# Performance work log

Hardware: AMD Instinct MI355X
Metric: run time of the kernel (lower is better)

Reference implementation:

```python
import jax, jax.numpy as jnp
import numpy as np

B, N, DIM, H, DH, P = 4, 4096, 256, 8, 64, 2
INNER = H * DH  # 512


def setup_inputs() -> dict:
    key = jax.random.key(0)
    ks = jax.random.split(key, 10)
    w = lambda k, shape: jax.random.normal(k, shape, dtype=jnp.float32) * 0.02
    return dict(
        x=jax.random.normal(ks[0], (B, N, DIM), dtype=jnp.float32),
        prev_x=jax.random.normal(ks[1], (B, N, DIM), dtype=jnp.float32),
        ln_q_g=jnp.ones((2 * DIM,), jnp.float32), ln_q_b=jnp.zeros((2 * DIM,), jnp.float32),
        ln_k_g=jnp.ones((DIM,), jnp.float32), ln_k_b=jnp.zeros((DIM,), jnp.float32),
        ln_v_g=jnp.ones((DIM,), jnp.float32), ln_v_b=jnp.zeros((DIM,), jnp.float32),
        Wq=w(ks[2], (2 * DIM, INNER)),            # to_q, bias=False
        Wk=w(ks[3], (DIM, INNER)), bk=jnp.zeros((INNER,), jnp.float32),
        Wv=w(ks[4], (DIM, INNER)), bv=jnp.zeros((INNER,), jnp.float32),
        Woff=w(ks[5], (H * P, INNER)),            # 1x1 conv == linear over channels
        boff=jax.random.uniform(ks[6], (H * P,), jnp.float32, -1.0, 1.0),
        Wout=w(ks[7], (DIM, INNER)), bout=jnp.zeros((DIM,), jnp.float32),
    )


def _ln(x, g, b):
    m = x.mean(-1, keepdims=True)
    v = ((x - m) ** 2).mean(-1, keepdims=True)
    return (x - m) * jax.lax.rsqrt(v + 1e-5) * g + b


def reference(x, prev_x, ln_q_g, ln_q_b, ln_k_g, ln_k_b, ln_v_g, ln_v_b,
              Wq, Wk, bk, Wv, bv, Woff, boff, Wout, bout):
    scale = DH ** -0.5
    # queries from cat(x, prev_x) along feature dim
    q = _ln(jnp.concatenate([x, prev_x], axis=-1), ln_q_g, ln_q_b) @ Wq  # (B,N,INNER)
    # learned per-head, per-point offsets (1x1 conv over channels)
    offsets = (q @ Woff.T + boff).reshape(B, N, H, P).transpose(0, 2, 3, 1)  # (B,H,P,N)
    # K/V from cat(x, prev_x) along batch dim -> KV length 2N per (b,h)
    kv = jnp.concatenate([x, prev_x], axis=0)  # (2B,N,DIM)
    k = (_ln(kv, ln_k_g, ln_k_b) @ Wk + bk).reshape(2, B, N, H, DH).transpose(1, 3, 4, 0, 2).reshape(B, H, DH, 2 * N)
    v = (_ln(kv, ln_v_g, ln_v_b) @ Wv + bv).reshape(2, B, N, H, DH).transpose(1, 3, 4, 0, 2).reshape(B, H, DH, 2 * N)
    # sampling positions: pos + offset, clamped, truncated to int (matches torch .long())
    pos = jnp.arange(N, dtype=jnp.float32)
    samp = jnp.clip(pos[None, None, None, :] + offsets, 0, 2 * N - 1).astype(jnp.int32)  # (B,H,P,N)
    idx = samp.transpose(0, 1, 3, 2)[:, :, None, :, :]  # (B,H,1,N,P)
    k_s = jnp.take_along_axis(k[:, :, :, None, :], idx, axis=-1)  # (B,H,DH,N,P)
    v_s = jnp.take_along_axis(v[:, :, :, None, :], idx, axis=-1)  # (B,H,DH,N,P)
    qh = q.reshape(B, N, H, DH).transpose(0, 2, 1, 3) * scale     # (B,H,N,DH)
    sim = jnp.einsum('bhnd,bhdnp->bhnp', qh, k_s)                  # (B,H,N,P)
    attn = jax.nn.softmax(sim, axis=-1)
    out = jnp.einsum('bhnp,bhdnp->bhnd', attn, v_s)                # (B,H,N,DH)
    out = out.transpose(0, 2, 1, 3).reshape(B, N, INNER) @ Wout.T + bout  # (B,N,DIM)
    return out, offsets
```

## Files before the change

### kernel.cpp

```cpp
#include <hip/hip_runtime.h>
#include <hip/hip_bf16.h>
#include <math.h>

#define B_    4
#define N_    4096
#define DIM_  256
#define H_    8
#define DH_   64
#define P_    2
#define INNER_ 512
#define BN_   (B_ * N_)
#define KVR_  (2 * BN_)

typedef short v8s  __attribute__((ext_vector_type(8)));
typedef short v4s  __attribute__((ext_vector_type(4)));
typedef float v4f  __attribute__((ext_vector_type(4)));

__device__ __forceinline__ short f2b(float x) {
    __hip_bfloat16 h = __float2bfloat16(x);
    return *reinterpret_cast<short*>(&h);
}
__device__ __forceinline__ float b2f(short s) {
    __hip_bfloat16 h = *reinterpret_cast<__hip_bfloat16*>(&s);
    return __bfloat162float(h);
}

__device__ __forceinline__ void async16(const void* g, void* l) {
    __builtin_amdgcn_global_load_lds(
        (const __attribute__((address_space(1))) void*)g,
        (__attribute__((address_space(3))) void*)l, 16, 0, 0);
}

__device__ __forceinline__ void storeRow(float* p, float4 f0, float4 f1, float4 f2, float4 f3) {
    ((float4*)p)[0] = f0; ((float4*)p)[1] = f1; ((float4*)p)[2] = f2; ((float4*)p)[3] = f3;
}
__device__ __forceinline__ void storeRow(__hip_bfloat16* p, float4 f0, float4 f1, float4 f2, float4 f3) {
    v8s o0, o1;
    o0[0]=f2b(f0.x); o0[1]=f2b(f0.y); o0[2]=f2b(f0.z); o0[3]=f2b(f0.w);
    o0[4]=f2b(f1.x); o0[5]=f2b(f1.y); o0[6]=f2b(f1.z); o0[7]=f2b(f1.w);
    o1[0]=f2b(f2.x); o1[1]=f2b(f2.y); o1[2]=f2b(f2.z); o1[3]=f2b(f2.w);
    o1[4]=f2b(f3.x); o1[5]=f2b(f3.y); o1[6]=f2b(f3.z); o1[7]=f2b(f3.w);
    ((v8s*)p)[0] = o0; ((v8s*)p)[1] = o1;
}

__global__ __launch_bounds__(256) void prep_all(
    const float* __restrict__ Wq, const float* __restrict__ gq, const float* __restrict__ betaq,
    const float* __restrict__ Wk, const float* __restrict__ gk, const float* __restrict__ betak,
    const float* __restrict__ bk,
    const float* __restrict__ Wv, const float* __restrict__ gv, const float* __restrict__ betav,
    const float* __restrict__ bv,
    const float* __restrict__ Woff, const float* __restrict__ Wout,
    short* __restrict__ Wq2t, float* __restrict__ bq2,
    short* __restrict__ Wkvt, float* __restrict__ bkv,
    float* __restrict__ Wcomb, float* __restrict__ braw, short* __restrict__ Woutb) {
    __shared__ float sm[272];
    const int bid = blockIdx.x, t = threadIdx.x;

    if (bid < 1536) {
        const float *W, *g, *beta, *bias_in;
        short* Wt; float* b2; int K, n; float scale;
        if (bid < 512)       { W=Wq; g=gq; beta=betaq; bias_in=nullptr; Wt=Wq2t; b2=bq2; K=512; n=bid;        scale=0.125f; }
        else if (bid < 1024) { W=Wk; g=gk; beta=betak; bias_in=bk; Wt=Wkvt;           b2=bkv;       K=256; n=bid-512;  scale=1.f; }
        else                 { W=Wv; g=gv; beta=betav; bias_in=bv; Wt=Wkvt+512*256;   b2=bkv+512;   K=256; n=bid-1024; scale=1.f; }
        float partial = 0.f;
        for (int k = t; k < K; k += 256) {
            float w = W[k * 512 + n];
            Wt[(size_t)n * K + k] = f2b(scale * g[k] * w);
            partial += beta[k] * w;
        }
        sm[t] = partial;
        __syncthreads();
        for (int s = 128; s > 0; s >>= 1) {
            if (t < s) sm[t] += sm[t + s];
            __syncthreads();
        }
        if (t == 0) b2[n] = scale * ((bias_in ? bias_in[n] : 0.f) + sm[0]);
    } else if (bid < 2048) {
        const int k = bid - 1536;
        const int hp = t & 15, jg = t >> 4;
        float p = 0.f;
        for (int j = jg; j < INNER_; j += 16)
            p += Wq[k * INNER_ + j] * Woff[hp * INNER_ + j];
        sm[jg * 17 + hp] = p;
        __syncthreads();
        if (t < 16) {
            float s = 0.f;
            for (int i = 0; i < 16; i++) s += sm[i * 17 + t];
            Wcomb[k * 16 + t] = gq[k] * s;
            braw[k * 16 + t]  = betaq[k] * s;
        }
    } else {
        const int i0 = (bid - 2048) * 1024 + t * 4;
        float4 f = *(const float4*)(Wout + i0);
        v4s o;
        o[0] = f2b(f.x); o[1] = f2b(f.y); o[2] = f2b(f.z); o[3] = f2b(f.w);
        *(v4s*)(Woutb + i0) = o;
    }
}

__global__ void bcomb_sum(const float* __restrict__ braw, const float* __restrict__ boff,
                          float* __restrict__ bcomb) {
    __shared__ float sm[272];
    int t = threadIdx.x;
    int hp = t & 15, kg = t >> 4;
    float p = 0.f;
    for (int k = kg; k < 512; k += 16) p += braw[k * 16 + hp];
    sm[kg * 17 + hp] = p;
    __syncthreads();
    if (t < 16) {
        float s = 0.f;
        for (int i = 0; i < 16; i++) s += sm[i * 17 + t];
        bcomb[t] = s + boff[t];
    }
}

__global__ __launch_bounds__(256) void norm_fused_kernel(
    const float* __restrict__ x, const float* __restrict__ p,
    const float* __restrict__ Wcomb, const float* __restrict__ bcomb,
    short* __restrict__ Aq, short* __restrict__ Akv,
    float* __restrict__ out_off, int* __restrict__ idx) {
    const int lane = threadIdx.x & 63;
    const int wv   = threadIdx.x >> 6;
    const int m0   = (blockIdx.x * 4 + wv) * 4;
    const int k8   = lane * 8;

    float4 w[8][4];
#pragma unroll
    for (int i = 0; i < 8; i++) {
        const float4* wr = (const float4*)(Wcomb + (size_t)(k8 + i) * 16);
#pragma unroll
        for (int j = 0; j < 4; j++) w[i][j] = wr[j];
    }
    const float bc = bcomb[lane & 15];

    const float* srcb = (lane < 32) ? (x + k8) : (p + k8 - DIM_);

    float4 u0 = ((const float4*)(srcb + (size_t)m0 * DIM_))[0];
    float4 u1 = ((const float4*)(srcb + (size_t)m0 * DIM_))[1];

#pragma unroll
    for (int r = 0; r < 4; r++) {
        const int m = m0 + r;
        float4 n0, n1;
        if (r < 3) {
            n0 = ((const float4*)(srcb + (size_t)(m + 1) * DIM_))[0];
            n1 = ((const float4*)(srcb + (size_t)(m + 1) * DIM_))[1];
        }
        float uv[8] = { u0.x, u0.y, u0.z, u0.w, u1.x, u1.y, u1.z, u1.w };

        float s = 0.f, q2 = 0.f;
#pragma unroll
        for (int i = 0; i < 8; i++) { s += uv[i]; q2 += uv[i] * uv[i]; }
#pragma unroll
        for (int d = 1; d <= 16; d <<= 1) {
            s  += __shfl_xor(s, d);
            q2 += __shfl_xor(q2, d);
        }
        float mean_h = s * (1.f / 256.f);
        float var_h  = q2 * (1.f / 256.f) - mean_h * mean_h;
        float rstd_h = rsqrtf(var_h + 1e-5f);
        float sf  = s  + __shfl_xor(s, 32);
        float q2f = q2 + __shfl_xor(q2, 32);
        float mean_q = sf * (1.f / 512.f);
        float var_q  = q2f * (1.f / 512.f) - mean_q * mean_q;
        float rstd_q = rsqrtf(var_q + 1e-5f);

        v8s okv;
#pragma unroll
        for (int i = 0; i < 8; i++) okv[i] = f2b((uv[i] - mean_h) * rstd_h);
        short* akvdst = Akv + ((lane < 32) ? ((size_t)m * DIM_ + k8)
                                           : ((size_t)(BN_ + m) * DIM_ + k8 - DIM_));
        *(v8s*)akvdst = okv;

        float nv[8];
        v8s oq;
#pragma unroll
        for (int i = 0; i < 8; i++) { nv[i] = (uv[i] - mean_q) * rstd_q; oq[i] = f2b(nv[i]); }
        *(v8s*)(Aq + (size_t)m * INNER_ + k8) = oq;

        float acc[16];
#pragma unroll
        for (int h = 0; h < 16; h++) acc[h] = 0.f;
#pragma unroll
        for (int i = 0; i < 8; i++) {
            float nvi = nv[i];
            acc[0]  += nvi * w[i][0].x;  acc[1]  += nvi * w[i][0].y;
            acc[2]  += nvi * w[i][0].z;  acc[3]  += nvi * w[i][0].w;
            acc[4]  += nvi * w[i][1].x;  acc[5]  += nvi * w[i][1].y;
            acc[6]  += nvi * w[i][1].z;  acc[7]  += nvi * w[i][1].w;
            acc[8]  += nvi * w[i][2].x;  acc[9]  += nvi * w[i][2].y;
            acc[10] += nvi * w[i][2].z;  acc[11] += nvi * w[i][2].w;
            acc[12] += nvi * w[i][3].x;  acc[13] += nvi * w[i][3].y;
            acc[14] += nvi * w[i][3].z;  acc[15] += nvi * w[i][3].w;
        }
        float a8[8];
#pragma unroll
        for (int j = 0; j < 8; j++) {
            float lo = acc[2 * j] + __shfl_xor(acc[2 * j], 1);
            float hi = acc[2 * j + 1] + __shfl_xor(acc[2 * j + 1], 1);
            a8[j] = (lane & 1) ? hi : lo;
        }
        float a4[4];
#pragma unroll
        for (int j = 0; j < 4; j++) {
            float lo = a8[2 * j] + __shfl_xor(a8[2 * j], 2);
            float hi = a8[2 * j + 1] + __shfl_xor(a8[2 * j + 1], 2);
            a4[j] = (lane & 2) ? hi : lo;
        }
        float a2[2];
#pragma unroll
        for (int j = 0; j < 2; j++) {
            float lo = a4[2 * j] + __shfl_xor(a4[2 * j], 4);
            float hi = a4[2 * j + 1] + __shfl_xor(a4[2 * j + 1], 4);
            a2[j] = (lane & 4) ? hi : lo;
        }
        float l1 = a2[0] + __shfl_xor(a2[0], 8);
        float h1 = a2[1] + __shfl_xor(a2[1], 8);
        float a1 = (lane & 8) ? h1 : l1;
        a1 += __shfl_xor(a1, 16);
        a1 += __shfl_xor(a1, 32);

        if (lane < 16) {
            float off = a1 + bc;
            int b = m >> 12, n = m & (N_ - 1);
            int h = lane >> 1, pp = lane & 1;
            out_off[(size_t)((b * H_ + h) * P_ + pp) * N_ + n] = off;
            float f = fminf(fmaxf((float)n + off, 0.f), (float)(2 * N_ - 1));
            idx[((size_t)(b * H_ + h) * N_ + n) * P_ + pp] = (int)f;
        }
        u0 = n0; u1 = n1;
    }
}

template <typename OT>
__device__ __forceinline__ void gemm_body(
    short* smem, const short* __restrict__ A, const short* __restrict__ Bt,
    const float* __restrict__ bias, OT* __restrict__ C, int N, int K, int nx, int lin) {
    short* As = smem;
    short* Bs = smem + 128 * 64;
    const int tid  = threadIdx.x;
    const int lane = tid & 63, w = tid >> 6;
    const int wr = w >> 1, wc = w & 1;
    const int lm = lane & 15, g = lane >> 4;

    const int x8 = lin & 7, t = lin >> 3;
    const int bx = t % nx, by = (t / nx) * 8 + x8;
    const int row0 = by * 128, col0 = bx * 128;

    const short* pa[4];
    const short* pb[4];
#pragma unroll
    for (int r = 0; r < 4; r++) {
        int s   = tid + 256 * r;
        int row = s >> 3, kcs = s & 7;
        int kg  = kcs ^ (row & 7);
        pa[r] = A  + (size_t)(row0 + row) * K + kg * 8;
        pb[r] = Bt + (size_t)(col0 + row) * K + kg * 8;
    }

    v4f acc[4][4];
#pragma unroll
    for (int i = 0; i < 4; i++)
#pragma unroll
        for (int j = 0; j < 4; j++) acc[i][j] = (v4f){0.f, 0.f, 0.f, 0.f};

    for (int k0 = 0; k0 < K; k0 += 64) {
        __syncthreads();
#pragma unroll
        for (int r = 0; r < 4; r++) {
            int s = tid + 256 * r;
            async16(pa[r] + k0, (char*)As + s * 16);
            async16(pb[r] + k0, (char*)Bs + s * 16);
        }
        __syncthreads();
#pragma unroll
        for (int ks = 0; ks < 2; ks++) {
            v8s af[4], bf[4];
#pragma unroll
            for (int i = 0; i < 4; i++) {
                int m   = wr * 64 + i * 16 + lm;
                int sch = m * 8 + ((ks * 4 + g) ^ (m & 7));
                af[i] = *(const v8s*)(As + sch * 8);
            }
#pragma unroll
            for (int j = 0; j < 4; j++) {
                int n   = wc * 64 + j * 16 + lm;
                int sch = n * 8 + ((ks * 4 + g) ^ (n & 7));
                bf[j] = *(const v8s*)(Bs + sch * 8);
            }
#pragma unroll
            for (int i = 0; i < 4; i++)
#pragma unroll
                for (int j = 0; j < 4; j++)
                    acc[i][j] = __builtin_amdgcn_mfma_f32_16x16x32_bf16(af[i], bf[j], acc[i][j], 0, 0, 0);
        }
    }

#pragma unroll
    for (int j = 0; j < 4; j++) {
        int gc = col0 + wc * 64 + j * 16 + lm;
        float bj = bias ? bias[gc] : 0.f;
#pragma unroll
        for (int i = 0; i < 4; i++)
#pragma unroll
            for (int r = 0; r < 4; r++) acc[i][j][r] += bj;
    }

    __syncthreads();
    float* ep = (float*)smem + w * (16 * 68);
#pragma unroll
    for (int i = 0; i < 4; i++) {
#pragma unroll
        for (int j = 0; j < 4; j++)
#pragma unroll
            for (int r = 0; r < 4; r++)
                ep[(g * 4 + r) * 68 + j * 16 + lm] = acc[i][j][r];
        asm volatile("s_waitcnt lgkmcnt(0)" ::: "memory");
        int rr = lane >> 2, cb = (lane & 3) * 16;
        float4 f0 = *(float4*)(ep + rr * 68 + cb + 0);
        float4 f1 = *(float4*)(ep + rr * 68 + cb + 4);
        float4 f2 = *(float4*)(ep + rr * 68 + cb + 8);
        float4 f3 = *(float4*)(ep + rr * 68 + cb + 12);
        asm volatile("s_waitcnt lgkmcnt(0)" ::: "memory");
        int grow = row0 + wr * 64 + i * 16 + rr;
        int gcol = col0 + wc * 64 + cb;
        storeRow(&C[(size_t)grow * N + gcol], f0, f1, f2, f3);
    }
}

__global__ __launch_bounds__(256) void gemm_qkv(
    const short* __restrict__ Aq, const short* __restrict__ Wq2t,
    const float* __restrict__ bq2, __hip_bfloat16* __restrict__ qb,
    const short* __restrict__ Akv, const short* __restrict__ Wkvt,
    const float* __restrict__ bkv, __hip_bfloat16* __restrict__ kvproj) {
    __shared__ short smem[2 * 128 * 64];
    const int bid = blockIdx.x;
    if (bid < 512)
        gemm_body<__hip_bfloat16>(smem, Aq, Wq2t, bq2, qb, 512, 512, 4, bid);
    else
        gemm_body<__hip_bfloat16>(smem, Akv, Wkvt, bkv, kvproj, 1024, 256, 8, bid - 512);
}

__global__ __launch_bounds__(256) void gemm_out(
    const short* __restrict__ A, const short* __restrict__ Bt,
    const float* __restrict__ bias, float* __restrict__ C) {
    __shared__ short smem[2 * 128 * 64];
    const int lin = blockIdx.y * gridDim.x + blockIdx.x;
    gemm_body<float>(smem, A, Bt, bias, C, 256, 512, 2, lin);
}

__global__ __launch_bounds__(256) void attn_kernel(
    const short* __restrict__ qb, const short* __restrict__ kvproj,
    const int* __restrict__ idx, short* __restrict__ attnout) {
    const int lane = threadIdx.x & 63;
    const int wv   = threadIdx.x >> 6;
    const int s    = lane >> 4, c = lane & 15;
    const int n = blockIdx.x * 16 + wv * 4 + s;
    const int h = blockIdx.y, b = blockIdx.z;
    const int m = b * N_ + n;

    v4s qv = *(const v4s*)(qb + (size_t)m * INNER_ + h * DH_ + c * 4);

    const int* ip = idx + ((size_t)(b * H_ + h) * N_ + n) * P_;
    int j0 = ip[0], j1 = ip[1];
    int r0 = b * N_ + j0 + ((j0 >= N_) ? (BN_ - N_) : 0);
    int r1 = b * N_ + j1 + ((j1 >= N_) ? (BN_ - N_) : 0);
    const short* k0p = kvproj + (size_t)r0 * 1024 + h * DH_ + c * 4;
    const short* k1p = kvproj + (size_t)r1 * 1024 + h * DH_ + c * 4;
    v4s k0 = *(const v4s*)k0p, v0 = *(const v4s*)(k0p + 512);
    v4s k1 = *(const v4s*)k1p, v1 = *(const v4s*)(k1p + 512);

    float q0 = b2f(qv[0]), q1 = b2f(qv[1]), q2 = b2f(qv[2]), q3 = b2f(qv[3]);
    float s0 = q0 * b2f(k0[0]) + q1 * b2f(k0[1]) + q2 * b2f(k0[2]) + q3 * b2f(k0[3]);
    float s1 = q0 * b2f(k1[0]) + q1 * b2f(k1[1]) + q2 * b2f(k1[2]) + q3 * b2f(k1[3]);
#pragma unroll
    for (int d = 1; d <= 8; d <<= 1) {
        s0 += __shfl_xor(s0, d);
        s1 += __shfl_xor(s1, d);
    }
    float mx = fmaxf(s0, s1);
    float e0 = __expf(s0 - mx), e1 = __expf(s1 - mx);
    float inv = 1.f / (e0 + e1);
    v4s o;
#pragma unroll
    for (int i = 0; i < 4; i++)
        o[i] = f2b((e0 * b2f(v0[i]) + e1 * b2f(v1[i])) * inv);
    *(v4s*)(attnout + (size_t)m * INNER_ + h * DH_ + c * 4) = o;
}

extern "C" void kernel_launch(void* const* d_in, const int* in_sizes, int n_in,
                              void* d_out, int out_size, void* d_ws, size_t ws_size,
                              hipStream_t stream) {
    (void)in_sizes; (void)n_in; (void)out_size; (void)ws_size;

    const float* x      = (const float*)d_in[0];
    const float* prevx  = (const float*)d_in[1];
    const float* ln_q_g = (const float*)d_in[2];
    const float* ln_q_b = (const float*)d_in[3];
    const float* ln_k_g = (const float*)d_in[4];
    const float* ln_k_b = (const float*)d_in[5];
    const float* ln_v_g = (const float*)d_in[6];
    const float* ln_v_b = (const float*)d_in[7];
    const float* Wq     = (const float*)d_in[8];
    const float* Wk     = (const float*)d_in[9];
    const float* bk     = (const float*)d_in[10];
    const float* Wv     = (const float*)d_in[11];
    const float* bv     = (const float*)d_in[12];
    const float* Woff   = (const float*)d_in[13];
    const float* boff   = (const float*)d_in[14];
    const float* Wout   = (const float*)d_in[15];
    const float* bout   = (const float*)d_in[16];

    char* cur = (char*)d_ws;
    auto alloc = [&](size_t bytes) { char* p = cur; cur += (bytes + 255) & ~(size_t)255; return p; };
    short* Aq      = (short*)alloc((size_t)BN_ * INNER_ * 2);
    short* Akv     = (short*)alloc((size_t)KVR_ * DIM_ * 2);
    short* qb      = (short*)alloc((size_t)BN_ * INNER_ * 2);
    short* kvproj  = (short*)alloc((size_t)KVR_ * 1024 * 2);
    short* attnout = (short*)alloc((size_t)BN_ * INNER_ * 2);
    short* Wq2t    = (short*)alloc(512 * 512 * 2);
    short* Wkvt    = (short*)alloc(1024 * 256 * 2);
    short* Woutb   = (short*)alloc(256 * 512 * 2);
    float* bq2     = (float*)alloc(512 * 4);
    float* bkv     = (float*)alloc(1024 * 4);
    float* Wcomb   = (float*)alloc(512 * 16 * 4);
    float* braw    = (float*)alloc(512 * 16 * 4);
    float* bcomb   = (float*)alloc(16 * 4);
    int*   idxb    = (int*)alloc((size_t)BN_ * 16 * 4);

    float* out_main = (float*)d_out;
    float* out_off  = out_main + (size_t)BN_ * DIM_;

    prep_all<<<2176, 256, 0, stream>>>(Wq, ln_q_g, ln_q_b,
                                       Wk, ln_k_g, ln_k_b, bk,
                                       Wv, ln_v_g, ln_v_b, bv,
                                       Woff, Wout,
                                       Wq2t, bq2, Wkvt, bkv, Wcomb, braw, Woutb);
    bcomb_sum<<<1, 256, 0, stream>>>(braw, boff, bcomb);

    norm_fused_kernel<<<BN_ / 16, 256, 0, stream>>>(x, prevx, Wcomb, bcomb,
                                                    Aq, Akv, out_off, idxb);

    gemm_qkv<<<2560, 256, 0, stream>>>(Aq, Wq2t, bq2, (__hip_bfloat16*)qb,
                                       Akv, Wkvt, bkv, (__hip_bfloat16*)kvproj);

    dim3 ga(N_ / 16, H_, B_);
    attn_kernel<<<ga, 256, 0, stream>>>(qb, kvproj, idxb, attnout);

    gemm_out<<<dim3(2, 128), 256, 0, stream>>>(attnout, Woutb, bout, out_main);
}
```

Baseline: 220.4 us.

## Replace QKV GEMM with 256x256-tile, 512-thread ping-pong pipelined kernel

Swaps the 128x128-tile fused QKV GEMM for a 256x256-tile kernel with 8 waves, double-buffered async LDS staging split into quarter stages interleaved with MFMA quadrants, plus an XCD-aware tile remap. Larger tiles raise arithmetic intensity and cut global reloads of A and B. The staged barriers aim to overlap loads with MFMA work. In exchange it uses 128KB of LDS and more accumulator registers per block and launches fewer blocks (640), so occupancy and tail effects could hurt.

```diff
diff --git a/kernel.cpp b/kernel.cpp
--- a/kernel.cpp
+++ b/kernel.cpp
@@ -328,17 +328,157 @@
     }
 }
 
-__global__ __launch_bounds__(256) void gemm_qkv(
-    const short* __restrict__ Aq, const short* __restrict__ Wq2t,
+#define ATILE_ (256 * 64)
+
+__global__ __launch_bounds__(512, 2) void gemm_qkv_256(
+    const short* __restrict__ Aqp, const short* __restrict__ Wq2t,
     const float* __restrict__ bq2, __hip_bfloat16* __restrict__ qb,
-    const short* __restrict__ Akv, const short* __restrict__ Wkvt,
+    const short* __restrict__ Akvp, const short* __restrict__ Wkvt,
     const float* __restrict__ bkv, __hip_bfloat16* __restrict__ kvproj) {
-    __shared__ short smem[2 * 128 * 64];
-    const int bid = blockIdx.x;
-    if (bid < 512)
-        gemm_body<__hip_bfloat16>(smem, Aq, Wq2t, bq2, qb, 512, 512, 4, bid);
-    else
-        gemm_body<__hip_bfloat16>(smem, Akv, Wkvt, bkv, kvproj, 1024, 256, 8, bid - 512);
+    __shared__ short smem[4 * ATILE_];
+
+    const short* A; const short* Bt; const float* bias; __hip_bfloat16* C;
+    int N, K, NT, nxs, nwg, lin;
+    if ((int)blockIdx.x < 128) {
+        A = Aqp;  Bt = Wq2t; bias = bq2; C = qb;
+        N = 512;  K = 512; NT = 8; nxs = 1; nwg = 128; lin = blockIdx.x;
+    } else {
+        A = Akvp; Bt = Wkvt; bias = bkv; C = kvproj;
+        N = 1024; K = 256; NT = 4; nxs = 2; nwg = 512; lin = blockIdx.x - 128;
+    }
+
+    const int tid  = threadIdx.x;
+    const int lane = tid & 63, w = tid >> 6;
+    const int wr = w >> 2, wc = w & 3;
+    const int lm = lane & 15, g = lane >> 4;
+
+    const int wg = (lin & 7) * (nwg >> 3) + (lin >> 3);
+    const int bx = wg & ((1 << nxs) - 1), by = wg >> nxs;
+    const int row0 = by << 8, col0 = bx << 8;
+
+    short* As0 = smem;
+    short* Bs0 = smem + 2 * ATILE_;
+
+    const int kg = ((tid & 7) ^ ((tid >> 3) & 7)) << 3;
+    const short* gA = A  + (size_t)(row0 + (tid >> 3)) * K + kg;
+    const short* gB = Bt + (size_t)(col0 + (tid >> 3)) * K + kg;
+
+    auto stage = [&](int buf, int k0, int which) {
+        const short* gp; char* lp;
+        if (which < 2) { gp = gA + (size_t)which * 128 * K;
+                         lp = (char*)(As0 + buf * ATILE_) + which * 16384; }
+        else           { gp = gB + (size_t)(which - 2) * 128 * K;
+                         lp = (char*)(Bs0 + buf * ATILE_) + (which - 2) * 16384; }
+        async16(gp + k0,                  lp + tid * 16);
+        async16(gp + k0 + (size_t)64 * K, lp + 8192 + tid * 16);
+    };
+
+    v4f acc[8][4];
+#pragma unroll
+    for (int i = 0; i < 8; i++)
+#pragma unroll
+        for (int j = 0; j < 4; j++) acc[i][j] = (v4f){0.f, 0.f, 0.f, 0.f};
+
+    float bj[4];
+#pragma unroll
+    for (int jj = 0; jj < 4; jj++) bj[jj] = bias[col0 + wc * 64 + jj * 16 + lm];
+
+    v8s aF[4][2];
+    v8s bF0[2][2], bF1[2][2];
+
+    auto RD_A = [&](const short* base, int qi) {
+#pragma unroll
+        for (int i = 0; i < 4; i++) {
+            const int m = wr * 128 + qi * 64 + i * 16 + lm;
+#pragma unroll
+            for (int ks = 0; ks < 2; ks++)
+                aF[i][ks] = *(const v8s*)(base + m * 64 + (((ks << 2) | g) ^ (m & 7)) * 8);
+        }
+    };
+    auto RD_B = [&](const short* base, int qj, v8s (*bf)[2]) {
+#pragma unroll
+        for (int j = 0; j < 2; j++) {
+            const int n = wc * 64 + qj * 32 + j * 16 + lm;
+#pragma unroll
+            for (int ks = 0; ks < 2; ks++)
+                bf[j][ks] = *(const v8s*)(base + n * 64 + (((ks << 2) | g) ^ (n & 7)) * 8);
+        }
+    };
+    auto MFMA_Q = [&](int qi, int qj, v8s (*bf)[2]) {
+        __builtin_amdgcn_s_setprio(1);
+#pragma unroll
+        for (int i = 0; i < 4; i++)
+#pragma unroll
+            for (int j = 0; j < 2; j++) {
+                acc[qi*4+i][qj*2+j] = __builtin_amdgcn_mfma_f32_16x16x32_bf16(aF[i][0], bf[j][0], acc[qi*4+i][qj*2+j], 0, 0, 0);
+                acc[qi*4+i][qj*2+j] = __builtin_amdgcn_mfma_f32_16x16x32_bf16(aF[i][1], bf[j][1], acc[qi*4+i][qj*2+j], 0, 0, 0);
+            }
+        __builtin_amdgcn_s_setprio(0);
+    };
+
+    stage(0, 0, 2); stage(0, 0, 3); stage(0, 0, 0); stage(0, 0, 1);
+    stage(1, 64, 2); stage(1, 64, 3);
+    asm volatile("s_waitcnt vmcnt(4)" ::: "memory");
+    __builtin_amdgcn_s_barrier();
+    asm volatile("" ::: "memory");
+
+    for (int T = 0; T < NT; ++T) {
+        const int cur = T & 1;
+        const short* as = As0 + cur * ATILE_;
+        const short* bs = Bs0 + cur * ATILE_;
+        const bool sA = (T + 1 < NT);
+        const bool sB = (T + 2 < NT);
+        const int kA = (T + 1) << 6, kB = (T + 2) << 6;
+
+        RD_A(as, 0); RD_B(bs, 0, bF0);
+        if (sA) stage(cur ^ 1, kA, 0);
+        __builtin_amdgcn_s_barrier();
+        asm volatile("s_waitcnt lgkmcnt(0)" ::: "memory");
+        MFMA_Q(0, 0, bF0);
+        __builtin_amdgcn_s_barrier();
+
+        RD_B(bs, 1, bF1);
+        if (sA) stage(cur ^ 1, kA, 1);
+        __builtin_amdgcn_s_barrier();
+        asm volatile("s_waitcnt lgkmcnt(0)" ::: "memory");
+        MFMA_Q(0, 1, bF1);
+        __builtin_amdgcn_s_barrier();
+
+        RD_A(as, 1);
+        if (sB) stage(cur, kB, 2);
+        __builtin_amdgcn_s_barrier();
+        asm volatile("s_waitcnt lgkmcnt(0)" ::: "memory");
+        MFMA_Q(1, 1, bF1);
+        __builtin_amdgcn_s_barrier();
+
+        if (sB) stage(cur, kB, 3);
+        __builtin_amdgcn_s_barrier();
+        MFMA_Q(1, 0, bF0);
+        if (sB)      asm volatile("s_waitcnt vmcnt(4)" ::: "memory");
+        else if (sA) asm volatile("s_waitcnt vmcnt(0)" ::: "memory");
+        __builtin_amdgcn_s_barrier();
+        asm volatile("" ::: "memory");
+    }
+
+    float* ep = (float*)smem + w * (16 * 68);
+#pragma unroll
+    for (int ii = 0; ii < 8; ii++) {
+#pragma unroll
+        for (int jj = 0; jj < 4; jj++)
+#pragma unroll
+            for (int r = 0; r < 4; r++)
+                ep[(g * 4 + r) * 68 + jj * 16 + lm] = acc[ii][jj][r] + bj[jj];
+        asm volatile("s_waitcnt lgkmcnt(0)" ::: "memory");
+        const int rr = lane >> 2, cb = (lane & 3) * 16;
+        float4 f0 = *(float4*)(ep + rr * 68 + cb + 0);
+        float4 f1 = *(float4*)(ep + rr * 68 + cb + 4);
+        float4 f2 = *(float4*)(ep + rr * 68 + cb + 8);
+        float4 f3 = *(float4*)(ep + rr * 68 + cb + 12);
+        asm volatile("s_waitcnt lgkmcnt(0)" ::: "memory");
+        const int grow = row0 + wr * 128 + ii * 16 + rr;
+        const int gcol = col0 + wc * 64 + cb;
+        storeRow(&C[(size_t)grow * N + gcol], f0, f1, f2, f3);
+    }
 }
 
 __global__ __launch_bounds__(256) void gemm_out(
@@ -441,8 +581,8 @@
     norm_fused_kernel<<<BN_ / 16, 256, 0, stream>>>(x, prevx, Wcomb, bcomb,
                                                     Aq, Akv, out_off, idxb);
 
-    gemm_qkv<<<2560, 256, 0, stream>>>(Aq, Wq2t, bq2, (__hip_bfloat16*)qb,
-                                       Akv, Wkvt, bkv, (__hip_bfloat16*)kvproj);
+    gemm_qkv_256<<<640, 512, 0, stream>>>(Aq, Wq2t, bq2, (__hip_bfloat16*)qb,
+                                          Akv, Wkvt, bkv, (__hip_bfloat16*)kvproj);
 
     dim3 ga(N_ / 16, H_, B_);
     attn_kernel<<<ga, 256, 0, stream>>>(qb, kvproj, idxb, attnout);
```

After: 218.1 us. No clear change (-1.1%).

## Double-buffer A tile in LDS and load B fragments directly from global

Applied to the files above, without the earlier changes.

The GEMM main loop now double-buffers the A tile in shared memory, prefetching the next K-slice asynchronously while MFMAs run on the current one, which cuts the barriers per iteration from two to one. B fragments are no longer staged through LDS; each lane reads its weight fragment straight from global memory into registers. This is meant to overlap loads with compute and reduce LDS traffic. In exchange, B reads go uncoalesced through the cache, global-load latency is exposed inside the loop, and register pressure rises.

```diff
diff --git a/kernel.cpp b/kernel.cpp
--- a/kernel.cpp
+++ b/kernel.cpp
@@ -236,8 +236,6 @@
 __device__ __forceinline__ void gemm_body(
     short* smem, const short* __restrict__ A, const short* __restrict__ Bt,
     const float* __restrict__ bias, OT* __restrict__ C, int N, int K, int nx, int lin) {
-    short* As = smem;
-    short* Bs = smem + 128 * 64;
     const int tid  = threadIdx.x;
     const int lane = tid & 63, w = tid >> 6;
     const int wr = w >> 1, wc = w & 1;
@@ -247,16 +245,21 @@
     const int bx = t % nx, by = (t / nx) * 8 + x8;
     const int row0 = by * 128, col0 = bx * 128;
 
+    short* As[2] = { smem, smem + 128 * 64 };
+
     const short* pa[4];
-    const short* pb[4];
 #pragma unroll
     for (int r = 0; r < 4; r++) {
         int s   = tid + 256 * r;
         int row = s >> 3, kcs = s & 7;
         int kg  = kcs ^ (row & 7);
-        pa[r] = A  + (size_t)(row0 + row) * K + kg * 8;
-        pb[r] = Bt + (size_t)(col0 + row) * K + kg * 8;
-    }
+        pa[r] = A + (size_t)(row0 + row) * K + kg * 8;
+    }
+
+    const short* pb[4];
+#pragma unroll
+    for (int j = 0; j < 4; j++)
+        pb[j] = Bt + (size_t)(col0 + wc * 64 + j * 16 + lm) * K + g * 8;
 
     v4f acc[4][4];
 #pragma unroll
@@ -264,36 +267,45 @@
 #pragma unroll
         for (int j = 0; j < 4; j++) acc[i][j] = (v4f){0.f, 0.f, 0.f, 0.f};
 
-    for (int k0 = 0; k0 < K; k0 += 64) {
-        __syncthreads();
-#pragma unroll
-        for (int r = 0; r < 4; r++) {
-            int s = tid + 256 * r;
-            async16(pa[r] + k0, (char*)As + s * 16);
-            async16(pb[r] + k0, (char*)Bs + s * 16);
-        }
-        __syncthreads();
+#pragma unroll
+    for (int r = 0; r < 4; r++)
+        async16(pa[r], (char*)As[0] + (tid + 256 * r) * 16);
+    __syncthreads();
+
+    const int NT = K >> 6;
+    for (int T = 0; T < NT; ++T) {
+        const int cur = T & 1;
+        const int k0 = T << 6;
+
+        v8s bfr[4][2];
+#pragma unroll
+        for (int j = 0; j < 4; j++)
+#pragma unroll
+            for (int ks = 0; ks < 2; ks++)
+                bfr[j][ks] = *(const v8s*)(pb[j] + k0 + ks * 32);
+
+        if (T + 1 < NT) {
+#pragma unroll
+            for (int r = 0; r < 4; r++)
+                async16(pa[r] + k0 + 64, (char*)As[cur ^ 1] + (tid + 256 * r) * 16);
+        }
+
 #pragma unroll
         for (int ks = 0; ks < 2; ks++) {
-            v8s af[4], bf[4];
+            v8s af[4];
 #pragma unroll
             for (int i = 0; i < 4; i++) {
                 int m   = wr * 64 + i * 16 + lm;
                 int sch = m * 8 + ((ks * 4 + g) ^ (m & 7));
-                af[i] = *(const v8s*)(As + sch * 8);
+                af[i] = *(const v8s*)(As[cur] + sch * 8);
             }
 #pragma unroll
-            for (int j = 0; j < 4; j++) {
-                int n   = wc * 64 + j * 16 + lm;
-                int sch = n * 8 + ((ks * 4 + g) ^ (n & 7));
-                bf[j] = *(const v8s*)(Bs + sch * 8);
-            }
-#pragma unroll
             for (int i = 0; i < 4; i++)
 #pragma unroll
                 for (int j = 0; j < 4; j++)
-                    acc[i][j] = __builtin_amdgcn_mfma_f32_16x16x32_bf16(af[i], bf[j], acc[i][j], 0, 0, 0);
-        }
+                    acc[i][j] = __builtin_amdgcn_mfma_f32_16x16x32_bf16(af[i], bfr[j][ks], acc[i][j], 0, 0, 0);
+        }
+        __syncthreads();
     }
 
 #pragma unroll
@@ -306,7 +318,6 @@
             for (int r = 0; r < 4; r++) acc[i][j][r] += bj;
     }
 
-    __syncthreads();
     float* ep = (float*)smem + w * (16 * 68);
 #pragma unroll
     for (int i = 0; i < 4; i++) {
```

After: 251.2 us. 13.9% more time.
